# Performance work log

Hardware: AMD Instinct MI355X
Metric: run time of the kernel (lower is better)

The kernel has to match this reference:

```python
import jax, jax.numpy as jnp
import numpy as np

B, N, U, K = 2, 768, 64, 8
IN = 2 * U + K  # 136
SLOPE = 0.01    # torch LeakyReLU default


def setup_inputs() -> dict:
    key = jax.random.key(0)
    ks = jax.random.split(key, 12)
    seq_embed = jax.random.normal(ks[0], (B, N, U), dtype=jnp.float32)
    vals = jax.random.uniform(ks[1], (N, N, K), dtype=jnp.float32)
    edge = (jax.random.uniform(ks[2], (N, N)) < 0.05) | jnp.eye(N, dtype=bool)
    relational_encoding = vals * edge[:, :, None].astype(jnp.float32)
    s = 0.05
    inp = {"seq_embed": seq_embed, "relational_encoding": relational_encoding}
    # per-hop MLP params: hop k has Linear(IN,IN) then Linear(IN,1); W stored (in,out)
    inp["w1_1"] = jax.random.normal(ks[3], (IN, IN), dtype=jnp.float32) * s
    inp["b1_1"] = jax.random.normal(ks[4], (IN,), dtype=jnp.float32) * s
    inp["w1_2"] = jax.random.normal(ks[5], (IN, 1), dtype=jnp.float32) * s
    inp["b1_2"] = jax.random.normal(ks[6], (1,), dtype=jnp.float32) * s
    inp["w2_1"] = jax.random.normal(ks[7], (IN, IN), dtype=jnp.float32) * s
    inp["b2_1"] = jax.random.normal(ks[8], (IN,), dtype=jnp.float32) * s
    inp["w2_2"] = jax.random.normal(ks[9], (IN, 1), dtype=jnp.float32) * s
    inp["b2_2"] = jax.random.normal(ks[10], (1,), dtype=jnp.float32) * s
    return inp


def _fwd(seq_embed, relational_encoding, hop_params):
    mask = (relational_encoding.sum(-1) > 0).astype(seq_embed.dtype)  # (N,N)
    D = mask.sum(-1)  # (N,) row degree
    rel = relational_encoding[None]  # (1,N,N,K) broadcast over batch
    x = seq_embed
    for layers in hop_params:
        b, n, u = x.shape
        e_i = jnp.broadcast_to(x[:, :, None, :], (b, n, n, u))  # row embed
        e_j = jnp.broadcast_to(x[:, None, :, :], (b, n, n, u))  # col embed
        seq_combined = jnp.concatenate([e_i, e_j], axis=-1)     # (B,N,N,2U)
        combined = jnp.concatenate(
            [seq_combined, jnp.broadcast_to(rel, (b, n, n, rel.shape[-1]))], axis=-1)
        combined = combined * mask[None, :, :, None]
        w = combined
        for (W, bb) in layers:
            w = jax.nn.leaky_relu(w @ W + bb, SLOPE)
        w = w[..., 0] * mask[None]                 # (B,N,N)
        scaled = w / D[None, :, None]              # divide each row i by D[i]
        # weighted neighbor embeds = scaled * e_j, summed over dim 1 (rows)
        x = jnp.einsum('bij,biju->bju', scaled, e_j)
    return x


def reference(seq_embed, relational_encoding, w1_1, b1_1, w1_2, b1_2,
              w2_1, b2_1, w2_2, b2_2):
    hop_params = [[(w1_1, b1_1), (w1_2, b1_2)], [(w2_1, b2_1), (w2_2, b2_2)]]
    return _fwd(seq_embed, relational_encoding, hop_params)
```

## Files before the change

### kernel.cpp

```cpp
#include <hip/hip_runtime.h>

#define NN 768
#define UU 64
#define KK 8
#define INF 136
#define BB 2
#define SLOPE 0.01f
#define CAP 80
#define NSLOT (NN*CAP)
#define NP 4
#define PSTRIDE 1552

__device__ __forceinline__ float lrelu(float x) { return x > 0.f ? x : SLOPE * x; }


__device__ __forceinline__ void pre_rows(int r4, const float* __restrict__ x,
                                         const float* __restrict__ W,
                                         float* __restrict__ A, float* __restrict__ Bv,
                                         float (*xs)[UU], int tid) {
    { int rr = tid >> 6, u = tid & 63;
      xs[rr][u] = x[(size_t)(r4 + rr) * UU + u]; }
    __syncthreads();
    int m = tid;
    if (m < INF) {
        float a[4] = {0.f,0.f,0.f,0.f}, bv[4] = {0.f,0.f,0.f,0.f};
        for (int u = 0; u < UU; u++) {
            float wa = W[u * INF + m];
            float wb = W[(UU + u) * INF + m];
#pragma unroll
            for (int r = 0; r < 4; r++) { a[r] += xs[r][u] * wa; bv[r] += xs[r][u] * wb; }
        }
#pragma unroll
        for (int r = 0; r < 4; r++) {
            A [(size_t)(r4 + r) * INF + m] = a[r];
            Bv[(size_t)(r4 + r) * INF + m] = bv[r];
        }
    }
}

__global__ void __launch_bounds__(256) k_setup(
        const float* __restrict__ rel, const float* __restrict__ seq,
        const float* __restrict__ W1, const float* __restrict__ W2,
        int* __restrict__ recs, int* __restrict__ rowcnt,
        float* __restrict__ A, float* __restrict__ Bv,
        float* __restrict__ P2, float* __restrict__ Q2,
        float* __restrict__ s1p, float* __restrict__ s2p) {
    __shared__ float xs[4][UU];
    __shared__ int wcnt[4];
    int blk = blockIdx.x;
    int tid = threadIdx.x;

    if (blk >= NN) {
        int g = blk - NN;
        bool h2 = g >= 384;
        if (h2) g -= 384;
        float* z = h2 ? s2p : s1p;
        int zi = g * 256 + tid;
        if (zi < NP * PSTRIDE) z[zi] = 0.f;
        pre_rows(g * 4, seq, h2 ? W2 : W1, h2 ? P2 : A, h2 ? Q2 : Bv, xs, tid);
        return;
    }

    int i = blk;
    int w = tid >> 6, lane = tid & 63;
    int j0 = w * 192;
    float sums[3];
#pragma unroll
    for (int it = 0; it < 3; it++) {
        int j = j0 + it * 64 + lane;
        const float4* rp = (const float4*)(rel + (size_t)(i * NN + j) * KK);
        float4 a = rp[0], b = rp[1];
        sums[it] = a.x + a.y + a.z + a.w + b.x + b.y + b.z + b.w;
    }
    int cnt = 0;
    int pos[3];
    bool act[3];
#pragma unroll
    for (int it = 0; it < 3; it++) {
        act[it] = sums[it] > 0.f;
        unsigned long long m = __ballot(act[it]);
        pos[it] = cnt + __popcll(m & ((1ull << lane) - 1));
        cnt += __popcll(m);
    }
    if (lane == 0) wcnt[w] = cnt;
    __syncthreads();
    int prefix = 0, total = 0;
#pragma unroll
    for (int ww = 0; ww < 4; ww++) {
        int c = wcnt[ww];
        total += c;
        if (ww < w) prefix += c;
    }
    if (tid == 0) rowcnt[i] = total < CAP ? total : CAP;
#pragma unroll
    for (int it = 0; it < 3; it++) {
        if (act[it]) {
            int rp = prefix + pos[it];
            if (rp < CAP) recs[i * CAP + rp] = j0 + it * 64 + lane;
        }
    }
}

template<bool H2>
__global__ void __launch_bounds__(256) k_hop(
        const int* __restrict__ recs, const int* __restrict__ rowcnt,
        const float* __restrict__ Ar, const float* __restrict__ Br,
        const float* __restrict__ rel, const float* __restrict__ W1,
        const float* __restrict__ b1, const float* __restrict__ w2,
        const float* __restrict__ b2, const float* __restrict__ sc,
        float* __restrict__ sp) {
    int lane = threadIdx.x & 63;
    int wid = (blockIdx.x * blockDim.x + threadIdx.x) >> 6;
    int i = wid / (CAP / 4);
    int w0 = (wid - i * (CAP / 4)) * 4;
    int cnt = rowcnt[i];
    if (w0 >= cnt) return;

    int hl = lane & 31, b = lane >> 5;
    int e0 = hl, e1 = 32 + hl, e2 = 64 + hl, e3 = 96 + hl, e4 = 128 + (hl & 7);

    const float* W1R = W1 + 128 * INF;
    float wr0[8], wr1[8], wr2[8], wr3[8], wr4[8];
#pragma unroll
    for (int k = 0; k < 8; k++) {
        const float* Wk = W1R + k * INF;
        wr0[k] = Wk[e0]; wr1[k] = Wk[e1]; wr2[k] = Wk[e2]; wr3[k] = Wk[e3]; wr4[k] = Wk[e4];
    }
    float bb0 = b1[e0], bb1 = b1[e1], bb2 = b1[e2], bb3 = b1[e3], bb4 = b1[e4];
    float w20 = w2[e0], w21 = w2[e1], w22 = w2[e2], w23 = w2[e3];
    float w24 = (hl < 8) ? w2[e4] : 0.f;
    float b2v = b2[0];
    float di = 1.0f / (float)cnt;

    const float* Ai = Ar + ((size_t)b * NN + i) * INF;
    float ai0 = Ai[e0], ai1 = Ai[e1], ai2 = Ai[e2], ai3 = Ai[e3], ai4 = Ai[e4];
    if (H2) {
        float si = 0.f;
#pragma unroll
        for (int p = 0; p < NP; p++) si += sc[p * PSTRIDE + b * NN + i];
        ai0 *= si; ai1 *= si; ai2 *= si; ai3 *= si; ai4 *= si;
    }

    float* s = sp + (wid & (NP - 1)) * PSTRIDE + b * NN;

    int4 q = *(const int4*)(recs + i * CAP + w0);
    int jj[4] = {q.x, q.y, q.z, q.w};
    int nt = cnt - w0;

#pragma unroll
    for (int t = 0; t < 4; t++) {
        if (t >= nt) break;
        int j = jj[t];
        const float* relp = rel + ((size_t)i * NN + j) * KK;
        float4 ra = ((const float4*)relp)[0];
        float4 rb = ((const float4*)relp)[1];
        float rv[8] = {ra.x, ra.y, ra.z, ra.w, rb.x, rb.y, rb.z, rb.w};
        float r0 = bb0, r1 = bb1, r2 = bb2, r3 = bb3, r4 = bb4;
#pragma unroll
        for (int k = 0; k < 8; k++) {
            r0 += rv[k] * wr0[k]; r1 += rv[k] * wr1[k]; r2 += rv[k] * wr2[k];
            r3 += rv[k] * wr3[k]; r4 += rv[k] * wr4[k];
        }
        const float* Bj = Br + ((size_t)b * NN + j) * INF;
        float sj = 1.f;
        if (H2) {
            sj = 0.f;
#pragma unroll
            for (int p = 0; p < NP; p++) sj += sc[p * PSTRIDE + b * NN + j];
        }
        float dot = lrelu(r0 + ai0 + sj * Bj[e0]) * w20
                  + lrelu(r1 + ai1 + sj * Bj[e1]) * w21
                  + lrelu(r2 + ai2 + sj * Bj[e2]) * w22
                  + lrelu(r3 + ai3 + sj * Bj[e3]) * w23
                  + lrelu(r4 + ai4 + sj * Bj[e4]) * w24;
#pragma unroll
        for (int off = 16; off; off >>= 1) dot += __shfl_xor(dot, off, 64);
        if (hl == 0) atomicAdd(&s[j], lrelu(dot + b2v) * di);
    }
}

__global__ void __launch_bounds__(256) k_final(const float4* __restrict__ seq,
                                               const float* __restrict__ s1p,
                                               const float* __restrict__ s2p,
                                               float4* __restrict__ out) {
    int idx = blockIdx.x * blockDim.x + threadIdx.x;
    int bj = idx >> 4;
    float f1 = 0.f, f2 = 0.f;
#pragma unroll
    for (int p = 0; p < NP; p++) { f1 += s1p[p * PSTRIDE + bj]; f2 += s2p[p * PSTRIDE + bj]; }
    float f = f1 * f2;
    float4 v = seq[idx];
    v.x *= f; v.y *= f; v.z *= f; v.w *= f;
    out[idx] = v;
}

extern "C" void kernel_launch(void* const* d_in, const int* in_sizes, int n_in,
                              void* d_out, int out_size, void* d_ws, size_t ws_size,
                              hipStream_t stream) {
    const float* seq  = (const float*)d_in[0];
    const float* rel  = (const float*)d_in[1];
    const float* w1_1 = (const float*)d_in[2];
    const float* b1_1 = (const float*)d_in[3];
    const float* w1_2 = (const float*)d_in[4];
    const float* b1_2 = (const float*)d_in[5];
    const float* w2_1 = (const float*)d_in[6];
    const float* b2_1 = (const float*)d_in[7];
    const float* w2_2 = (const float*)d_in[8];
    const float* b2_2 = (const float*)d_in[9];
    float* out = (float*)d_out;

    char* ws = (char*)d_ws;
    float* s1p   = (float*)(ws + 0);
    float* s2p   = (float*)(ws + 24832);
    int* rowcnt  = (int*)  (ws + 49664);
    float* A     = (float*)(ws + 52736);
    float* Bv    = (float*)(ws + 888320);
    float* P2    = (float*)(ws + 1723904);
    float* Q2    = (float*)(ws + 2559488);
    int* recs    = (int*)  (ws + 3395072);

    k_setup<<<NN + 768, 256, 0, stream>>>(rel, seq, w1_1, w2_1, recs, rowcnt,
                                          A, Bv, P2, Q2, s1p, s2p);
    k_hop<false><<<NSLOT / 16, 256, 0, stream>>>(recs, rowcnt, A, Bv, rel,
                                                 w1_1, b1_1, w1_2, b1_2, nullptr, s1p);
    k_hop<true><<<NSLOT / 16, 256, 0, stream>>>(recs, rowcnt, P2, Q2, rel,
                                                w2_1, b2_1, w2_2, b2_2, s1p, s2p);
    k_final<<<BB * NN * UU / 4 / 256, 256, 0, stream>>>((const float4*)seq, s1p, s2p,
                                                        (float4*)out);
}
```

Baseline: 128.6 us.

## Compact active relation vectors in setup and process eight edges per wave

```diff
diff --git a/kernel.cpp b/kernel.cpp
--- a/kernel.cpp
+++ b/kernel.cpp
@@ -44,7 +44,8 @@
         int* __restrict__ recs, int* __restrict__ rowcnt,
         float* __restrict__ A, float* __restrict__ Bv,
         float* __restrict__ P2, float* __restrict__ Q2,
-        float* __restrict__ s1p, float* __restrict__ s2p) {
+        float* __restrict__ s1p, float* __restrict__ s2p,
+        float* __restrict__ relc) {
     __shared__ float xs[4][UU];
     __shared__ int wcnt[4];
     int blk = blockIdx.x;
@@ -64,13 +65,15 @@
     int i = blk;
     int w = tid >> 6, lane = tid & 63;
     int j0 = w * 192;
+    float4 ra4[3], rb4[3];
     float sums[3];
 #pragma unroll
     for (int it = 0; it < 3; it++) {
         int j = j0 + it * 64 + lane;
         const float4* rp = (const float4*)(rel + (size_t)(i * NN + j) * KK);
-        float4 a = rp[0], b = rp[1];
-        sums[it] = a.x + a.y + a.z + a.w + b.x + b.y + b.z + b.w;
+        ra4[it] = rp[0]; rb4[it] = rp[1];
+        sums[it] = ra4[it].x + ra4[it].y + ra4[it].z + ra4[it].w
+                 + rb4[it].x + rb4[it].y + rb4[it].z + rb4[it].w;
     }
     int cnt = 0;
     int pos[3];
@@ -96,7 +99,11 @@
     for (int it = 0; it < 3; it++) {
         if (act[it]) {
             int rp = prefix + pos[it];
-            if (rp < CAP) recs[i * CAP + rp] = j0 + it * 64 + lane;
+            if (rp < CAP) {
+                recs[i * CAP + rp] = j0 + it * 64 + lane;
+                float4* rc = (float4*)(relc + ((size_t)i * CAP + rp) * 8);
+                rc[0] = ra4[it]; rc[1] = rb4[it];
+            }
         }
     }
 }
@@ -104,17 +111,19 @@
 template<bool H2>
 __global__ void __launch_bounds__(256) k_hop(
         const int* __restrict__ recs, const int* __restrict__ rowcnt,
+        const float* __restrict__ relc,
         const float* __restrict__ Ar, const float* __restrict__ Br,
-        const float* __restrict__ rel, const float* __restrict__ W1,
-        const float* __restrict__ b1, const float* __restrict__ w2,
-        const float* __restrict__ b2, const float* __restrict__ sc,
-        float* __restrict__ sp) {
+        const float* __restrict__ W1, const float* __restrict__ b1,
+        const float* __restrict__ w2, const float* __restrict__ b2,
+        const float* __restrict__ sc, float* __restrict__ sp) {
     int lane = threadIdx.x & 63;
     int wid = (blockIdx.x * blockDim.x + threadIdx.x) >> 6;
-    int i = wid / (CAP / 4);
-    int w0 = (wid - i * (CAP / 4)) * 4;
+    const int WPR = CAP / 8;
+    int i = wid / WPR;
+    int w0 = (wid - i * WPR) * 8;
     int cnt = rowcnt[i];
     if (w0 >= cnt) return;
+    int nt = cnt - w0; if (nt > 8) nt = 8;
 
     int hl = lane & 31, b = lane >> 5;
     int e0 = hl, e1 = 32 + hl, e2 = 64 + hl, e3 = 96 + hl, e4 = 128 + (hl & 7);
@@ -143,17 +152,17 @@
 
     float* s = sp + (wid & (NP - 1)) * PSTRIDE + b * NN;
 
-    int4 q = *(const int4*)(recs + i * CAP + w0);
-    int jj[4] = {q.x, q.y, q.z, q.w};
-    int nt = cnt - w0;
-
-#pragma unroll
-    for (int t = 0; t < 4; t++) {
+    int4 q0 = *(const int4*)(recs + i * CAP + w0);
+    int4 q1 = *(const int4*)(recs + i * CAP + w0 + 4);
+    int jj[8] = {q0.x, q0.y, q0.z, q0.w, q1.x, q1.y, q1.z, q1.w};
+    const float4* rc = (const float4*)(relc + ((size_t)i * CAP + w0) * 8);
+
+#pragma unroll
+    for (int t = 0; t < 8; t++) {
         if (t >= nt) break;
         int j = jj[t];
-        const float* relp = rel + ((size_t)i * NN + j) * KK;
-        float4 ra = ((const float4*)relp)[0];
-        float4 rb = ((const float4*)relp)[1];
+        float4 ra = rc[2 * t];
+        float4 rb = rc[2 * t + 1];
         float rv[8] = {ra.x, ra.y, ra.z, ra.w, rb.x, rb.y, rb.z, rb.w};
         float r0 = bb0, r1 = bb1, r2 = bb2, r3 = bb3, r4 = bb4;
 #pragma unroll
@@ -218,12 +227,13 @@
     float* P2    = (float*)(ws + 1723904);
     float* Q2    = (float*)(ws + 2559488);
     int* recs    = (int*)  (ws + 3395072);
+    float* relc  = (float*)(ws + 3640832);
 
     k_setup<<<NN + 768, 256, 0, stream>>>(rel, seq, w1_1, w2_1, recs, rowcnt,
-                                          A, Bv, P2, Q2, s1p, s2p);
-    k_hop<false><<<NSLOT / 16, 256, 0, stream>>>(recs, rowcnt, A, Bv, rel,
+                                          A, Bv, P2, Q2, s1p, s2p, relc);
+    k_hop<false><<<NSLOT / 32, 256, 0, stream>>>(recs, rowcnt, relc, A, Bv,
                                                  w1_1, b1_1, w1_2, b1_2, nullptr, s1p);
-    k_hop<true><<<NSLOT / 16, 256, 0, stream>>>(recs, rowcnt, P2, Q2, rel,
+    k_hop<true><<<NSLOT / 32, 256, 0, stream>>>(recs, rowcnt, relc, P2, Q2,
                                                 w2_1, b2_1, w2_2, b2_2, s1p, s2p);
     k_final<<<BB * NN * UU / 4 / 256, 256, 0, stream>>>((const float4*)seq, s1p, s2p,
                                                         (float4*)out);
```

Result: no change. 128.9 us (+0.2%).

## Switch hop kernels to column-owned gather, dropping edge lists, atomics and final kernel

Applied to the files above, without the earlier changes.

```diff
diff --git a/kernel.cpp b/kernel.cpp
--- a/kernel.cpp
+++ b/kernel.cpp
@@ -2,14 +2,9 @@
 
 #define NN 768
 #define UU 64
-#define KK 8
 #define INF 136
 #define BB 2
 #define SLOPE 0.01f
-#define CAP 80
-#define NSLOT (NN*CAP)
-#define NP 4
-#define PSTRIDE 1552
 
 __device__ __forceinline__ float lrelu(float x) { return x > 0.f ? x : SLOPE * x; }
 
@@ -41,10 +36,9 @@
 __global__ void __launch_bounds__(256) k_setup(
         const float* __restrict__ rel, const float* __restrict__ seq,
         const float* __restrict__ W1, const float* __restrict__ W2,
-        int* __restrict__ recs, int* __restrict__ rowcnt,
+        float* __restrict__ dinv,
         float* __restrict__ A, float* __restrict__ Bv,
-        float* __restrict__ P2, float* __restrict__ Q2,
-        float* __restrict__ s1p, float* __restrict__ s2p) {
+        float* __restrict__ P2, float* __restrict__ Q2) {
     __shared__ float xs[4][UU];
     __shared__ int wcnt[4];
     int blk = blockIdx.x;
@@ -54,9 +48,6 @@
         int g = blk - NN;
         bool h2 = g >= 384;
         if (h2) g -= 384;
-        float* z = h2 ? s2p : s1p;
-        int zi = g * 256 + tid;
-        if (zi < NP * PSTRIDE) z[zi] = 0.f;
         pre_rows(g * 4, seq, h2 ? W2 : W1, h2 ? P2 : A, h2 ? Q2 : Bv, xs, tid);
         return;
     }
@@ -64,134 +55,91 @@
     int i = blk;
     int w = tid >> 6, lane = tid & 63;
     int j0 = w * 192;
-    float sums[3];
+    int cnt = 0;
 #pragma unroll
     for (int it = 0; it < 3; it++) {
         int j = j0 + it * 64 + lane;
-        const float4* rp = (const float4*)(rel + (size_t)(i * NN + j) * KK);
+        const float4* rp = (const float4*)(rel + (size_t)(i * NN + j) * 8);
         float4 a = rp[0], b = rp[1];
-        sums[it] = a.x + a.y + a.z + a.w + b.x + b.y + b.z + b.w;
-    }
-    int cnt = 0;
-    int pos[3];
-    bool act[3];
-#pragma unroll
-    for (int it = 0; it < 3; it++) {
-        act[it] = sums[it] > 0.f;
-        unsigned long long m = __ballot(act[it]);
-        pos[it] = cnt + __popcll(m & ((1ull << lane) - 1));
-        cnt += __popcll(m);
+        float s = a.x + a.y + a.z + a.w + b.x + b.y + b.z + b.w;
+        cnt += __popcll(__ballot(s > 0.f));
     }
     if (lane == 0) wcnt[w] = cnt;
     __syncthreads();
-    int prefix = 0, total = 0;
-#pragma unroll
-    for (int ww = 0; ww < 4; ww++) {
-        int c = wcnt[ww];
-        total += c;
-        if (ww < w) prefix += c;
-    }
-    if (tid == 0) rowcnt[i] = total < CAP ? total : CAP;
-#pragma unroll
-    for (int it = 0; it < 3; it++) {
-        if (act[it]) {
-            int rp = prefix + pos[it];
-            if (rp < CAP) recs[i * CAP + rp] = j0 + it * 64 + lane;
-        }
-    }
+    if (tid == 0) dinv[i] = 1.0f / (float)(wcnt[0] + wcnt[1] + wcnt[2] + wcnt[3]);
 }
 
 template<bool H2>
 __global__ void __launch_bounds__(256) k_hop(
-        const int* __restrict__ recs, const int* __restrict__ rowcnt,
+        const float* __restrict__ rel, const float* __restrict__ dinv,
         const float* __restrict__ Ar, const float* __restrict__ Br,
-        const float* __restrict__ rel, const float* __restrict__ W1,
-        const float* __restrict__ b1, const float* __restrict__ w2,
-        const float* __restrict__ b2, const float* __restrict__ sc,
-        float* __restrict__ sp) {
+        const float* __restrict__ W, const float* __restrict__ b1,
+        const float* __restrict__ w2, const float* __restrict__ b2,
+        float* __restrict__ s1, const float* __restrict__ seq,
+        float* __restrict__ out) {
     int lane = threadIdx.x & 63;
     int wid = (blockIdx.x * blockDim.x + threadIdx.x) >> 6;
-    int i = wid / (CAP / 4);
-    int w0 = (wid - i * (CAP / 4)) * 4;
-    int cnt = rowcnt[i];
-    if (w0 >= cnt) return;
+    int b = wid >= NN ? 1 : 0;
+    int j = wid - b * NN;
 
-    int hl = lane & 31, b = lane >> 5;
-    int e0 = hl, e1 = 32 + hl, e2 = 64 + hl, e3 = 96 + hl, e4 = 128 + (hl & 7);
+    int e0 = lane, e1 = 64 + lane, e2 = 128 + (lane & 7);
 
-    const float* W1R = W1 + 128 * INF;
-    float wr0[8], wr1[8], wr2[8], wr3[8], wr4[8];
+    const float* WR = W + 128 * INF;
+    float wr0[8], wr1[8], wr2[8];
 #pragma unroll
     for (int k = 0; k < 8; k++) {
-        const float* Wk = W1R + k * INF;
-        wr0[k] = Wk[e0]; wr1[k] = Wk[e1]; wr2[k] = Wk[e2]; wr3[k] = Wk[e3]; wr4[k] = Wk[e4];
+        const float* Wk = WR + k * INF;
+        wr0[k] = Wk[e0]; wr1[k] = Wk[e1]; wr2[k] = Wk[e2];
     }
-    float bb0 = b1[e0], bb1 = b1[e1], bb2 = b1[e2], bb3 = b1[e3], bb4 = b1[e4];
-    float w20 = w2[e0], w21 = w2[e1], w22 = w2[e2], w23 = w2[e3];
-    float w24 = (hl < 8) ? w2[e4] : 0.f;
+    float bb0 = b1[e0], bb1 = b1[e1], bb2 = b1[e2];
+    float w20 = w2[e0], w21 = w2[e1], w22 = (lane < 8) ? w2[e2] : 0.f;
     float b2v = b2[0];
-    float di = 1.0f / (float)cnt;
 
-    const float* Ai = Ar + ((size_t)b * NN + i) * INF;
-    float ai0 = Ai[e0], ai1 = Ai[e1], ai2 = Ai[e2], ai3 = Ai[e3], ai4 = Ai[e4];
-    if (H2) {
-        float si = 0.f;
+    const float* Bj = Br + ((size_t)b * NN + j) * INF;
+    float bc0 = Bj[e0], bc1 = Bj[e1], bc2 = Bj[e2];
+    float sjj = 1.f;
+    if (H2) { sjj = s1[b * NN + j]; bc0 *= sjj; bc1 *= sjj; bc2 *= sjj; }
+
+    float acc = 0.f;
+    for (int r = 0; r < 12; r++) {
+        int ib = r * 64 + lane;
+        const float4* cp = (const float4*)(rel + ((size_t)ib * NN + j) * 8);
+        float4 ca = cp[0], cb = cp[1];
+        float sm = ca.x + ca.y + ca.z + ca.w + cb.x + cb.y + cb.z + cb.w;
+        unsigned long long m = __ballot(sm > 0.f);
+        while (m) {
+            int s = __ffsll((unsigned long long)m) - 1;
+            m &= m - 1;
+            int i = r * 64 + s;
+            float rv[8];
+            rv[0] = __shfl(ca.x, s, 64); rv[1] = __shfl(ca.y, s, 64);
+            rv[2] = __shfl(ca.z, s, 64); rv[3] = __shfl(ca.w, s, 64);
+            rv[4] = __shfl(cb.x, s, 64); rv[5] = __shfl(cb.y, s, 64);
+            rv[6] = __shfl(cb.z, s, 64); rv[7] = __shfl(cb.w, s, 64);
+            float r0 = bb0, r1 = bb1, r2 = bb2;
 #pragma unroll
-        for (int p = 0; p < NP; p++) si += sc[p * PSTRIDE + b * NN + i];
-        ai0 *= si; ai1 *= si; ai2 *= si; ai3 *= si; ai4 *= si;
+            for (int k = 0; k < 8; k++) {
+                r0 += rv[k] * wr0[k]; r1 += rv[k] * wr1[k]; r2 += rv[k] * wr2[k];
+            }
+            const float* Ai = Ar + ((size_t)b * NN + i) * INF;
+            float a0 = Ai[e0], a1 = Ai[e1], a2 = Ai[e2];
+            if (H2) { float si = s1[b * NN + i]; a0 *= si; a1 *= si; a2 *= si; }
+            float dot = lrelu(r0 + a0 + bc0) * w20
+                      + lrelu(r1 + a1 + bc1) * w21
+                      + lrelu(r2 + a2 + bc2) * w22;
+#pragma unroll
+            for (int off = 32; off; off >>= 1) dot += __shfl_xor(dot, off, 64);
+            acc += dinv[i] * lrelu(dot + b2v);
+        }
     }
 
-    float* s = sp + (wid & (NP - 1)) * PSTRIDE + b * NN;
-
-    int4 q = *(const int4*)(recs + i * CAP + w0);
-    int jj[4] = {q.x, q.y, q.z, q.w};
-    int nt = cnt - w0;
-
-#pragma unroll
-    for (int t = 0; t < 4; t++) {
-        if (t >= nt) break;
-        int j = jj[t];
-        const float* relp = rel + ((size_t)i * NN + j) * KK;
-        float4 ra = ((const float4*)relp)[0];
-        float4 rb = ((const float4*)relp)[1];
-        float rv[8] = {ra.x, ra.y, ra.z, ra.w, rb.x, rb.y, rb.z, rb.w};
-        float r0 = bb0, r1 = bb1, r2 = bb2, r3 = bb3, r4 = bb4;
-#pragma unroll
-        for (int k = 0; k < 8; k++) {
-            r0 += rv[k] * wr0[k]; r1 += rv[k] * wr1[k]; r2 += rv[k] * wr2[k];
-            r3 += rv[k] * wr3[k]; r4 += rv[k] * wr4[k];
-        }
-        const float* Bj = Br + ((size_t)b * NN + j) * INF;
-        float sj = 1.f;
-        if (H2) {
-            sj = 0.f;
-#pragma unroll
-            for (int p = 0; p < NP; p++) sj += sc[p * PSTRIDE + b * NN + j];
-        }
-        float dot = lrelu(r0 + ai0 + sj * Bj[e0]) * w20
-                  + lrelu(r1 + ai1 + sj * Bj[e1]) * w21
-                  + lrelu(r2 + ai2 + sj * Bj[e2]) * w22
-                  + lrelu(r3 + ai3 + sj * Bj[e3]) * w23
-                  + lrelu(r4 + ai4 + sj * Bj[e4]) * w24;
-#pragma unroll
-        for (int off = 16; off; off >>= 1) dot += __shfl_xor(dot, off, 64);
-        if (hl == 0) atomicAdd(&s[j], lrelu(dot + b2v) * di);
+    if (H2) {
+        float f = sjj * acc;
+        size_t base = ((size_t)b * NN + j) * UU;
+        out[base + lane] = seq[base + lane] * f;
+    } else {
+        if (lane == 0) s1[b * NN + j] = acc;
     }
-}
-
-__global__ void __launch_bounds__(256) k_final(const float4* __restrict__ seq,
-                                               const float* __restrict__ s1p,
-                                               const float* __restrict__ s2p,
-                                               float4* __restrict__ out) {
-    int idx = blockIdx.x * blockDim.x + threadIdx.x;
-    int bj = idx >> 4;
-    float f1 = 0.f, f2 = 0.f;
-#pragma unroll
-    for (int p = 0; p < NP; p++) { f1 += s1p[p * PSTRIDE + bj]; f2 += s2p[p * PSTRIDE + bj]; }
-    float f = f1 * f2;
-    float4 v = seq[idx];
-    v.x *= f; v.y *= f; v.z *= f; v.w *= f;
-    out[idx] = v;
 }
 
 extern "C" void kernel_launch(void* const* d_in, const int* in_sizes, int n_in,
@@ -210,21 +158,16 @@
     float* out = (float*)d_out;
 
     char* ws = (char*)d_ws;
-    float* s1p   = (float*)(ws + 0);
-    float* s2p   = (float*)(ws + 24832);
-    int* rowcnt  = (int*)  (ws + 49664);
-    float* A     = (float*)(ws + 52736);
-    float* Bv    = (float*)(ws + 888320);
-    float* P2    = (float*)(ws + 1723904);
-    float* Q2    = (float*)(ws + 2559488);
-    int* recs    = (int*)  (ws + 3395072);
+    float* dinv = (float*)(ws + 0);
+    float* s1   = (float*)(ws + 4096);
+    float* A    = (float*)(ws + 16384);
+    float* Bv   = (float*)(ws + 851968);
+    float* P2   = (float*)(ws + 1687552);
+    float* Q2   = (float*)(ws + 2523136);
 
-    k_setup<<<NN + 768, 256, 0, stream>>>(rel, seq, w1_1, w2_1, recs, rowcnt,
-                                          A, Bv, P2, Q2, s1p, s2p);
-    k_hop<false><<<NSLOT / 16, 256, 0, stream>>>(recs, rowcnt, A, Bv, rel,
-                                                 w1_1, b1_1, w1_2, b1_2, nullptr, s1p);
-    k_hop<true><<<NSLOT / 16, 256, 0, stream>>>(recs, rowcnt, P2, Q2, rel,
-                                                w2_1, b2_1, w2_2, b2_2, s1p, s2p);
-    k_final<<<BB * NN * UU / 4 / 256, 256, 0, stream>>>((const float4*)seq, s1p, s2p,
-                                                        (float4*)out);
+    k_setup<<<NN + 768, 256, 0, stream>>>(rel, seq, w1_1, w2_1, dinv, A, Bv, P2, Q2);
+    k_hop<false><<<384, 256, 0, stream>>>(rel, dinv, A, Bv,
+                                          w1_1, b1_1, w1_2, b1_2, s1, seq, out);
+    k_hop<true><<<384, 256, 0, stream>>>(rel, dinv, P2, Q2,
+                                         w2_1, b2_1, w2_2, b2_2, s1, seq, out);
 }
```

New measurement: 148.2 us. +15.2%, slower.
